# Performance work log

Hardware: AMD Instinct MI355X
Metric: run time of the kernel (lower is better)

The kernel has to match this reference:

```python
import jax, jax.numpy as jnp
import numpy as np

DIM = 512

def setup_inputs() -> dict:
    key = jax.random.key(0)
    ks = jax.random.split(key, 7)
    S = 8192
    scale = 1.0 / np.sqrt(DIM)
    x = jax.random.normal(ks[0], (S, DIM), dtype=jnp.float32)
    # torch.nn.Linear params: weight [out, in], bias [out]
    Wq = jax.random.uniform(ks[1], (DIM, DIM), jnp.float32, -scale, scale)
    bq = jax.random.uniform(ks[2], (DIM,), jnp.float32, -scale, scale)
    Wk = jax.random.uniform(ks[3], (DIM, DIM), jnp.float32, -scale, scale)
    bk = jax.random.uniform(ks[4], (DIM,), jnp.float32, -scale, scale)
    Wv = jax.random.uniform(ks[5], (DIM, DIM), jnp.float32, -scale, scale)
    bv = jax.random.uniform(ks[6], (DIM,), jnp.float32, -scale, scale)
    return {"x": x, "Wq": Wq, "bq": bq, "Wk": Wk, "bk": bk, "Wv": Wv, "bv": bv}

def reference(x, Wq, bq, Wk, bk, Wv, bv):
    S = x.shape[0]
    q = x @ Wq.T + bq  # [S, D]
    k = x @ Wk.T + bk
    v = x @ Wv.T + bv
    scores = (q @ k.T) / jnp.sqrt(jnp.asarray(DIM, x.dtype))  # [S, S]
    causal = jnp.tril(jnp.ones((S, S), dtype=bool))  # keep lower triangle incl. diag
    scores = jnp.where(causal, scores, -jnp.inf)
    attn_weights = jax.nn.softmax(scores, axis=-1)
    output = attn_weights @ v  # [S, D]
    return (output, attn_weights)
```

## Files before the change

### kernel.cpp

```cpp
#include <hip/hip_runtime.h>
#include <hip/hip_bf16.h>
#include <stdint.h>

#define S 8192
#define D 512
#define SCALE 0.044194173824159216f
#define KSPLIT 8

typedef __attribute__((ext_vector_type(8))) short short8;
typedef __attribute__((ext_vector_type(4))) float f32x4;

__device__ inline unsigned short f32_to_bf16(float f) {
    union { float f; uint32_t u; } v; v.f = f;
    uint32_t u = v.u;
    uint32_t r = (u + 0x7FFFu + ((u >> 16) & 1u)) >> 16;
    return (unsigned short)r;
}

__device__ inline uint2 pack4(float4 v) {
    uint2 p;
    p.x = (uint32_t)f32_to_bf16(v.x) | ((uint32_t)f32_to_bf16(v.y) << 16);
    p.y = (uint32_t)f32_to_bf16(v.z) | ((uint32_t)f32_to_bf16(v.w) << 16);
    return p;
}

__global__ __launch_bounds__(256) void k_convert(
    const float* __restrict__ x, const float* __restrict__ Wq,
    const float* __restrict__ Wk, const float* __restrict__ Wv,
    short* __restrict__ xb, short* __restrict__ Wb) {
    size_t i4 = (size_t)blockIdx.x * 256 + threadIdx.x;
    const size_t XN4 = (size_t)S * D / 4;
    if (i4 < XN4) {
        float4 v = reinterpret_cast<const float4*>(x)[i4];
        reinterpret_cast<uint2*>(xb)[i4] = pack4(v);
    } else {
        size_t j4 = i4 - XN4;
        size_t w = j4 >> 16;
        size_t rem = j4 & 65535;
        const float* src = (w == 0) ? Wq : ((w == 1) ? Wk : Wv);
        float4 v = reinterpret_cast<const float4*>(src)[rem];
        reinterpret_cast<uint2*>(Wb)[j4] = pack4(v);
    }
}

__device__ inline void stage_bf16(const short* __restrict__ src, int ld, short* dst, int t) {
#pragma unroll
    for (int j = 0; j < 2; j++) {
        int c = t + j * 256;
        int r = c >> 2;
        int kc = (c & 3) * 8;
        uint4 v = *reinterpret_cast<const uint4*>(&src[(size_t)r * ld + kc]);
        *reinterpret_cast<uint4*>(&dst[r * 32 + kc]) = v;
    }
}

__device__ inline void mfma_tile(const short* As, const short* Bs,
                                 f32x4 acc[4][4], int wr, int wc, int lane) {
    int rl = lane & 15;
    int kg = lane >> 4;
    short8 a[4], b[4];
#pragma unroll
    for (int m = 0; m < 4; m++)
        a[m] = *reinterpret_cast<const short8*>(&As[(wr * 64 + m * 16 + rl) * 32 + kg * 8]);
#pragma unroll
    for (int n = 0; n < 4; n++)
        b[n] = *reinterpret_cast<const short8*>(&Bs[(wc * 64 + n * 16 + rl) * 32 + kg * 8]);
#pragma unroll
    for (int m = 0; m < 4; m++)
#pragma unroll
        for (int n = 0; n < 4; n++)
            acc[m][n] = __builtin_amdgcn_mfma_f32_16x16x32_bf16(a[m], b[n], acc[m][n], 0, 0, 0);
}

__global__ __launch_bounds__(256) void k_qkv(
    const short* __restrict__ xb, const short* __restrict__ Wb,
    const float* __restrict__ bq, const float* __restrict__ bk,
    const float* __restrict__ bv, short* __restrict__ QKV) {
    __shared__ short As[128 * 32], Bs[128 * 32];
    int which = blockIdx.z;
    const short* W = Wb + (size_t)which * D * D;
    const float* bias = (which == 0) ? bq : ((which == 1) ? bk : bv);
    short* out = QKV + (size_t)which * S * D;
    int r0 = blockIdx.x * 128, c0 = blockIdx.y * 128;
    int t = threadIdx.x, lane = t & 63, w = t >> 6, wr = w >> 1, wc = w & 1;
    f32x4 acc[4][4];
#pragma unroll
    for (int m = 0; m < 4; m++)
#pragma unroll
        for (int n = 0; n < 4; n++)
#pragma unroll
            for (int j = 0; j < 4; j++) acc[m][n][j] = 0.0f;

    for (int kk = 0; kk < D; kk += 32) {
        __syncthreads();
        stage_bf16(xb + (size_t)r0 * D + kk, D, As, t);
        stage_bf16(W + (size_t)c0 * D + kk, D, Bs, t);
        __syncthreads();
        mfma_tile(As, Bs, acc, wr, wc, lane);
    }
    int rg = lane >> 4, cl = lane & 15;
#pragma unroll
    for (int m = 0; m < 4; m++)
#pragma unroll
        for (int n = 0; n < 4; n++) {
            int col = c0 + wc * 64 + n * 16 + cl;
            float b = bias[col];
#pragma unroll
            for (int j = 0; j < 4; j++) {
                int row = r0 + wr * 64 + m * 16 + rg * 4 + j;
                out[(size_t)row * D + col] = (short)f32_to_bf16(acc[m][n][j] + b);
            }
        }
}

__global__ __launch_bounds__(256) void k_transpose(const short* __restrict__ V,
                                                   short* __restrict__ Vt) {
    __shared__ short tile[64][65];
    int r0 = blockIdx.x * 64;
    int c0 = blockIdx.y * 64;
    int t = threadIdx.x;
#pragma unroll
    for (int j = 0; j < 16; j++) {
        int idx = t + j * 256;
        int r = idx >> 6, c = idx & 63;
        tile[r][c] = V[(size_t)(r0 + r) * D + c0 + c];
    }
    __syncthreads();
#pragma unroll
    for (int j = 0; j < 16; j++) {
        int idx = t + j * 256;
        int rr = idx >> 6, cc = idx & 63;
        Vt[(size_t)(c0 + rr) * S + r0 + cc] = tile[cc][rr];
    }
}

__global__ __launch_bounds__(256) void k_scores(const short* __restrict__ Qb,
                                                const short* __restrict__ Kb,
                                                float* __restrict__ attn) {
    int bj = blockIdx.x, bi = blockIdx.y;
    int r0 = bi * 128, c0 = bj * 128;
    int t = threadIdx.x;
    if (bj > bi) {
#pragma unroll
        for (int j = 0; j < 16; j++) {
            int c = t + j * 256;
            int r = c >> 5;
            int c4 = (c & 31) * 4;
            *reinterpret_cast<float4*>(&attn[(size_t)(r0 + r) * S + c0 + c4]) =
                make_float4(0.f, 0.f, 0.f, 0.f);
        }
        return;
    }
    __shared__ short As[128 * 32], Bs[128 * 32];
    int lane = t & 63, w = t >> 6, wr = w >> 1, wc = w & 1;
    f32x4 acc[4][4];
#pragma unroll
    for (int m = 0; m < 4; m++)
#pragma unroll
        for (int n = 0; n < 4; n++)
#pragma unroll
            for (int j = 0; j < 4; j++) acc[m][n][j] = 0.0f;

    for (int kk = 0; kk < D; kk += 32) {
        __syncthreads();
        stage_bf16(Qb + (size_t)r0 * D + kk, D, As, t);
        stage_bf16(Kb + (size_t)c0 * D + kk, D, Bs, t);
        __syncthreads();
        mfma_tile(As, Bs, acc, wr, wc, lane);
    }
    int rg = lane >> 4, cl = lane & 15;
#pragma unroll
    for (int m = 0; m < 4; m++)
#pragma unroll
        for (int n = 0; n < 4; n++) {
            int col = c0 + wc * 64 + n * 16 + cl;
#pragma unroll
            for (int j = 0; j < 4; j++) {
                int row = r0 + wr * 64 + m * 16 + rg * 4 + j;
                float v = acc[m][n][j] * SCALE;
                if (col > row) v = 0.0f;
                attn[(size_t)row * S + col] = v;
            }
        }
}

__global__ __launch_bounds__(256) void k_softmax(float* __restrict__ attn) {
    __shared__ float buf[S];
    __shared__ float red[16];
    int i = blockIdx.x;
    int t = threadIdx.x;
    int n = i + 1;
    float m = -__builtin_inff();
    for (int j = t; j < n; j += 256) {
        float v = attn[(size_t)i * S + j];
        buf[j] = v;
        m = fmaxf(m, v);
    }
#pragma unroll
    for (int o = 32; o > 0; o >>= 1) m = fmaxf(m, __shfl_xor(m, o, 64));
    int wid = t >> 6, lane = t & 63;
    if (lane == 0) red[wid] = m;
    __syncthreads();
    if (t == 0) {
        float mm = fmaxf(fmaxf(red[0], red[1]), fmaxf(red[2], red[3]));
        red[8] = mm;
    }
    __syncthreads();
    float M = red[8];
    float s = 0.f;
    for (int j = t; j < n; j += 256) {
        float e = __expf(buf[j] - M);
        buf[j] = e;
        s += e;
    }
#pragma unroll
    for (int o = 32; o > 0; o >>= 1) s += __shfl_xor(s, o, 64);
    __syncthreads();
    if (lane == 0) red[wid] = s;
    __syncthreads();
    if (t == 0) red[9] = 1.0f / (red[0] + red[1] + red[2] + red[3]);
    __syncthreads();
    float inv = red[9];
    for (int j = t; j < n; j += 256) attn[(size_t)i * S + j] = buf[j] * inv;
}

__global__ __launch_bounds__(256) void k_pv(const float* __restrict__ attn,
                                            const short* __restrict__ Vt,
                                            float* __restrict__ out) {
    int bn = blockIdx.x;
    int bi = blockIdx.y;
    int kz = blockIdx.z;
    int nsteps = (bi + 1) * 4;
    int per = (nsteps + KSPLIT - 1) / KSPLIT;
    int st0 = kz * per, st1 = min(nsteps, st0 + per);
    if (st0 >= st1) return;
    __shared__ short As[128 * 32], Bs[128 * 32];
    int r0 = bi * 128, c0 = bn * 128;
    int t = threadIdx.x, lane = t & 63, w = t >> 6, wr = w >> 1, wc = w & 1;
    f32x4 acc[4][4];
#pragma unroll
    for (int m = 0; m < 4; m++)
#pragma unroll
        for (int n = 0; n < 4; n++)
#pragma unroll
            for (int j = 0; j < 4; j++) acc[m][n][j] = 0.0f;

    for (int st = st0; st < st1; ++st) {
        int kk = st * 32;
        __syncthreads();
#pragma unroll
        for (int j = 0; j < 4; j++) {
            int c = t + j * 256;
            int r = c >> 3;
            int kc = (c & 7) * 4;
            float4 v = *reinterpret_cast<const float4*>(&attn[(size_t)(r0 + r) * S + kk + kc]);
            *reinterpret_cast<uint2*>(&As[r * 32 + kc]) = pack4(v);
        }
#pragma unroll
        for (int j = 0; j < 2; j++) {
            int c = t + j * 256;
            int r = c >> 2;
            int kc = (c & 3) * 8;
            uint4 v = *reinterpret_cast<const uint4*>(&Vt[(size_t)(c0 + r) * S + kk + kc]);
            *reinterpret_cast<uint4*>(&Bs[r * 32 + kc]) = v;
        }
        __syncthreads();
        mfma_tile(As, Bs, acc, wr, wc, lane);
    }
    int rg = lane >> 4, cl = lane & 15;
#pragma unroll
    for (int m = 0; m < 4; m++)
#pragma unroll
        for (int n = 0; n < 4; n++) {
            int col = c0 + wc * 64 + n * 16 + cl;
#pragma unroll
            for (int j = 0; j < 4; j++) {
                int row = r0 + wr * 64 + m * 16 + rg * 4 + j;
                atomicAdd(&out[(size_t)row * D + col], acc[m][n][j]);
            }
        }
}

extern "C" void kernel_launch(void* const* d_in, const int* in_sizes, int n_in,
                              void* d_out, int out_size, void* d_ws, size_t ws_size,
                              hipStream_t stream) {
    const float* x  = (const float*)d_in[0];
    const float* Wq = (const float*)d_in[1];
    const float* bq = (const float*)d_in[2];
    const float* Wk = (const float*)d_in[3];
    const float* bk = (const float*)d_in[4];
    const float* Wv = (const float*)d_in[5];
    const float* bv = (const float*)d_in[6];
    float* out  = (float*)d_out;
    float* attn = out + (size_t)S * D;

    short* xb  = (short*)d_ws;
    short* Wb  = xb + (size_t)S * D;
    short* QKV = Wb + (size_t)3 * D * D;
    short* Vt  = QKV + (size_t)3 * S * D;
    const short* Qb = QKV;
    const short* Kb = QKV + (size_t)S * D;
    const short* Vb = QKV + (size_t)2 * S * D;

    {
        size_t total4 = (size_t)S * D / 4 + (size_t)3 * D * D / 4;
        k_convert<<<dim3((unsigned)(total4 / 256)), 256, 0, stream>>>(x, Wq, Wk, Wv, xb, Wb);
    }
    k_qkv<<<dim3(S / 128, D / 128, 3), 256, 0, stream>>>(xb, Wb, bq, bk, bv, QKV);
    k_transpose<<<dim3(S / 64, D / 64), 256, 0, stream>>>(Vb, Vt);
    k_scores<<<dim3(S / 128, S / 128), 256, 0, stream>>>(Qb, Kb, attn);
    k_softmax<<<dim3(S), 256, 0, stream>>>(attn);
    hipMemsetAsync(d_out, 0, (size_t)S * D * sizeof(float), stream);
    k_pv<<<dim3(D / 128, S / 128, KSPLIT), 256, 0, stream>>>(attn, Vt, out);
}
```

Baseline: 575.3 us.

## Fuse softmax into scores and PV kernels using per-tile max/sum partials

```diff
diff --git a/kernel.cpp b/kernel.cpp
--- a/kernel.cpp
+++ b/kernel.cpp
@@ -5,7 +5,8 @@
 #define S 8192
 #define D 512
 #define SCALE 0.044194173824159216f
-#define KSPLIT 8
+#define KZ 4
+#define NEG_BIG -1e30f
 
 typedef __attribute__((ext_vector_type(8))) short short8;
 typedef __attribute__((ext_vector_type(4))) float f32x4;
@@ -22,6 +23,40 @@
     p.x = (uint32_t)f32_to_bf16(v.x) | ((uint32_t)f32_to_bf16(v.y) << 16);
     p.y = (uint32_t)f32_to_bf16(v.z) | ((uint32_t)f32_to_bf16(v.w) << 16);
     return p;
+}
+
+__device__ inline void gload16(const void* g, void* l) {
+    __builtin_amdgcn_global_load_lds(
+        (const __attribute__((address_space(1))) unsigned int*)g,
+        (__attribute__((address_space(3))) unsigned int*)l, 16, 0, 0);
+}
+
+__device__ inline void stage_g2l(const short* __restrict__ src, int ld, short* dst, int t) {
+    int w = t >> 6, l = t & 63;
+    int lr = l >> 2, lc = (l & 3) * 8;
+#pragma unroll
+    for (int j = 0; j < 2; j++) {
+        int row = (w << 5) + (j << 4) + lr;
+        gload16(src + (size_t)row * ld + lc, dst + (w << 10) + (j << 9));
+    }
+}
+
+__device__ inline void mfma_tile(const short* As, const short* Bs,
+                                 f32x4 acc[4][4], int wr, int wc, int lane) {
+    int rl = lane & 15;
+    int kg = lane >> 4;
+    short8 a[4], b[4];
+#pragma unroll
+    for (int m = 0; m < 4; m++)
+        a[m] = *reinterpret_cast<const short8*>(&As[(wr * 64 + m * 16 + rl) * 32 + kg * 8]);
+#pragma unroll
+    for (int n = 0; n < 4; n++)
+        b[n] = *reinterpret_cast<const short8*>(&Bs[(wc * 64 + n * 16 + rl) * 32 + kg * 8]);
+#pragma unroll
+    for (int m = 0; m < 4; m++)
+#pragma unroll
+        for (int n = 0; n < 4; n++)
+            acc[m][n] = __builtin_amdgcn_mfma_f32_16x16x32_bf16(a[m], b[n], acc[m][n], 0, 0, 0);
 }
 
 __global__ __launch_bounds__(256) void k_convert(
@@ -43,40 +78,11 @@
     }
 }
 
-__device__ inline void stage_bf16(const short* __restrict__ src, int ld, short* dst, int t) {
-#pragma unroll
-    for (int j = 0; j < 2; j++) {
-        int c = t + j * 256;
-        int r = c >> 2;
-        int kc = (c & 3) * 8;
-        uint4 v = *reinterpret_cast<const uint4*>(&src[(size_t)r * ld + kc]);
-        *reinterpret_cast<uint4*>(&dst[r * 32 + kc]) = v;
-    }
-}
-
-__device__ inline void mfma_tile(const short* As, const short* Bs,
-                                 f32x4 acc[4][4], int wr, int wc, int lane) {
-    int rl = lane & 15;
-    int kg = lane >> 4;
-    short8 a[4], b[4];
-#pragma unroll
-    for (int m = 0; m < 4; m++)
-        a[m] = *reinterpret_cast<const short8*>(&As[(wr * 64 + m * 16 + rl) * 32 + kg * 8]);
-#pragma unroll
-    for (int n = 0; n < 4; n++)
-        b[n] = *reinterpret_cast<const short8*>(&Bs[(wc * 64 + n * 16 + rl) * 32 + kg * 8]);
-#pragma unroll
-    for (int m = 0; m < 4; m++)
-#pragma unroll
-        for (int n = 0; n < 4; n++)
-            acc[m][n] = __builtin_amdgcn_mfma_f32_16x16x32_bf16(a[m], b[n], acc[m][n], 0, 0, 0);
-}
-
 __global__ __launch_bounds__(256) void k_qkv(
     const short* __restrict__ xb, const short* __restrict__ Wb,
     const float* __restrict__ bq, const float* __restrict__ bk,
     const float* __restrict__ bv, short* __restrict__ QKV) {
-    __shared__ short As[128 * 32], Bs[128 * 32];
+    __shared__ __align__(16) short As[128 * 32], Bs[128 * 32];
     int which = blockIdx.z;
     const short* W = Wb + (size_t)which * D * D;
     const float* bias = (which == 0) ? bq : ((which == 1) ? bk : bv);
@@ -93,8 +99,8 @@
 
     for (int kk = 0; kk < D; kk += 32) {
         __syncthreads();
-        stage_bf16(xb + (size_t)r0 * D + kk, D, As, t);
-        stage_bf16(W + (size_t)c0 * D + kk, D, Bs, t);
+        stage_g2l(xb + (size_t)r0 * D + kk, D, As, t);
+        stage_g2l(W + (size_t)c0 * D + kk, D, Bs, t);
         __syncthreads();
         mfma_tile(As, Bs, acc, wr, wc, lane);
     }
@@ -136,7 +142,10 @@
 
 __global__ __launch_bounds__(256) void k_scores(const short* __restrict__ Qb,
                                                 const short* __restrict__ Kb,
-                                                float* __restrict__ attn) {
+                                                float* __restrict__ raw,
+                                                float* __restrict__ attn,
+                                                float* __restrict__ pm,
+                                                float* __restrict__ pl) {
     int bj = blockIdx.x, bi = blockIdx.y;
     int r0 = bi * 128, c0 = bj * 128;
     int t = threadIdx.x;
@@ -151,7 +160,8 @@
         }
         return;
     }
-    __shared__ short As[128 * 32], Bs[128 * 32];
+    __shared__ __align__(16) short As[128 * 32], Bs[128 * 32];
+    __shared__ float wred[2][128], wsum[2][128];
     int lane = t & 63, w = t >> 6, wr = w >> 1, wc = w & 1;
     f32x4 acc[4][4];
 #pragma unroll
@@ -163,80 +173,103 @@
 
     for (int kk = 0; kk < D; kk += 32) {
         __syncthreads();
-        stage_bf16(Qb + (size_t)r0 * D + kk, D, As, t);
-        stage_bf16(Kb + (size_t)c0 * D + kk, D, Bs, t);
+        stage_g2l(Qb + (size_t)r0 * D + kk, D, As, t);
+        stage_g2l(Kb + (size_t)c0 * D + kk, D, Bs, t);
         __syncthreads();
         mfma_tile(As, Bs, acc, wr, wc, lane);
     }
     int rg = lane >> 4, cl = lane & 15;
+    bool diag = (bi == bj);
+#pragma unroll
+    for (int m = 0; m < 4; m++)
+#pragma unroll
+        for (int n = 0; n < 4; n++)
+#pragma unroll
+            for (int jj = 0; jj < 4; jj++) {
+                int row = wr * 64 + m * 16 + rg * 4 + jj;
+                int col = wc * 64 + n * 16 + cl;
+                float v = acc[m][n][jj] * SCALE;
+                if (diag && col > row) v = NEG_BIG;
+                acc[m][n][jj] = v;
+            }
+#pragma unroll
+    for (int m = 0; m < 4; m++)
+#pragma unroll
+        for (int jj = 0; jj < 4; jj++) {
+            float x = fmaxf(fmaxf(acc[m][0][jj], acc[m][1][jj]),
+                            fmaxf(acc[m][2][jj], acc[m][3][jj]));
+#pragma unroll
+            for (int o = 1; o < 16; o <<= 1) x = fmaxf(x, __shfl_xor(x, o, 64));
+            if (cl == 0) wred[wc][wr * 64 + m * 16 + rg * 4 + jj] = x;
+        }
+    __syncthreads();
+#pragma unroll
+    for (int m = 0; m < 4; m++)
+#pragma unroll
+        for (int jj = 0; jj < 4; jj++) {
+            int rloc = wr * 64 + m * 16 + rg * 4 + jj;
+            float mr = fmaxf(wred[0][rloc], wred[1][rloc]);
+            float sse = __expf(acc[m][0][jj] - mr) + __expf(acc[m][1][jj] - mr) +
+                        __expf(acc[m][2][jj] - mr) + __expf(acc[m][3][jj] - mr);
+#pragma unroll
+            for (int o = 1; o < 16; o <<= 1) sse += __shfl_xor(sse, o, 64);
+            if (cl == 0) wsum[wc][rloc] = sse;
+        }
 #pragma unroll
     for (int m = 0; m < 4; m++)
 #pragma unroll
         for (int n = 0; n < 4; n++) {
             int col = c0 + wc * 64 + n * 16 + cl;
 #pragma unroll
-            for (int j = 0; j < 4; j++) {
-                int row = r0 + wr * 64 + m * 16 + rg * 4 + j;
-                float v = acc[m][n][j] * SCALE;
-                if (col > row) v = 0.0f;
-                attn[(size_t)row * S + col] = v;
+            for (int jj = 0; jj < 4; jj++) {
+                int row = r0 + wr * 64 + m * 16 + rg * 4 + jj;
+                raw[(size_t)row * S + col] = acc[m][n][jj];
             }
         }
-}
-
-__global__ __launch_bounds__(256) void k_softmax(float* __restrict__ attn) {
-    __shared__ float buf[S];
-    __shared__ float red[16];
-    int i = blockIdx.x;
+    __syncthreads();
+    if (t < 128) {
+        float mr = fmaxf(wred[0][t], wred[1][t]);
+        pm[(size_t)bj * S + r0 + t] = mr;
+        pl[(size_t)bj * S + r0 + t] = wsum[0][t] + wsum[1][t];
+    }
+}
+
+__global__ __launch_bounds__(256) void k_combine(const float* __restrict__ pm,
+                                                 const float* __restrict__ pl,
+                                                 float* __restrict__ M,
+                                                 float* __restrict__ Li) {
+    int row = blockIdx.x * 256 + threadIdx.x;
+    int nt = (row >> 7) + 1;
+    float m = -3e38f;
+    for (int j = 0; j < nt; j++) m = fmaxf(m, pm[(size_t)j * S + row]);
+    float l = 0.f;
+    for (int j = 0; j < nt; j++) l += pl[(size_t)j * S + row] * __expf(pm[(size_t)j * S + row] - m);
+    M[row] = m;
+    Li[row] = 1.0f / l;
+}
+
+__global__ __launch_bounds__(512) void k_pvnorm(const float* __restrict__ raw,
+                                                const short* __restrict__ Vt,
+                                                const float* __restrict__ M,
+                                                const float* __restrict__ Li,
+                                                float* __restrict__ attn,
+                                                float* __restrict__ out) {
+    int idx = blockIdx.x;
+    int panel = 63 - (idx & 63);
+    int rest = idx >> 6;
+    int bn = rest & 1;
+    int kz = rest >> 1;
+    int r0 = panel * 128;
     int t = threadIdx.x;
-    int n = i + 1;
-    float m = -__builtin_inff();
-    for (int j = t; j < n; j += 256) {
-        float v = attn[(size_t)i * S + j];
-        buf[j] = v;
-        m = fmaxf(m, v);
-    }
-#pragma unroll
-    for (int o = 32; o > 0; o >>= 1) m = fmaxf(m, __shfl_xor(m, o, 64));
-    int wid = t >> 6, lane = t & 63;
-    if (lane == 0) red[wid] = m;
-    __syncthreads();
-    if (t == 0) {
-        float mm = fmaxf(fmaxf(red[0], red[1]), fmaxf(red[2], red[3]));
-        red[8] = mm;
-    }
-    __syncthreads();
-    float M = red[8];
-    float s = 0.f;
-    for (int j = t; j < n; j += 256) {
-        float e = __expf(buf[j] - M);
-        buf[j] = e;
-        s += e;
-    }
-#pragma unroll
-    for (int o = 32; o > 0; o >>= 1) s += __shfl_xor(s, o, 64);
-    __syncthreads();
-    if (lane == 0) red[wid] = s;
-    __syncthreads();
-    if (t == 0) red[9] = 1.0f / (red[0] + red[1] + red[2] + red[3]);
-    __syncthreads();
-    float inv = red[9];
-    for (int j = t; j < n; j += 256) attn[(size_t)i * S + j] = buf[j] * inv;
-}
-
-__global__ __launch_bounds__(256) void k_pv(const float* __restrict__ attn,
-                                            const short* __restrict__ Vt,
-                                            float* __restrict__ out) {
-    int bn = blockIdx.x;
-    int bi = blockIdx.y;
-    int kz = blockIdx.z;
-    int nsteps = (bi + 1) * 4;
-    int per = (nsteps + KSPLIT - 1) / KSPLIT;
-    int st0 = kz * per, st1 = min(nsteps, st0 + per);
+    int nst = (panel + 1) * 4;
+    int per = (nst + KZ - 1) / KZ;
+    int st0 = kz * per, st1 = min(nst, st0 + per);
     if (st0 >= st1) return;
-    __shared__ short As[128 * 32], Bs[128 * 32];
-    int r0 = bi * 128, c0 = bn * 128;
-    int t = threadIdx.x, lane = t & 63, w = t >> 6, wr = w >> 1, wc = w & 1;
+    __shared__ __align__(16) short As[128 * 32];
+    __shared__ __align__(16) short Bs[256 * 32];
+    __shared__ float Ml[128], Ll[128];
+    if (t < 128) { Ml[t] = M[r0 + t]; Ll[t] = Li[r0 + t]; }
+    int lane = t & 63, w = t >> 6, wr = w >> 2, wc = w & 3;
     f32x4 acc[4][4];
 #pragma unroll
     for (int m = 0; m < 4; m++)
@@ -245,25 +278,26 @@
 #pragma unroll
             for (int j = 0; j < 4; j++) acc[m][n][j] = 0.0f;
 
+    const short* vbase = Vt + (size_t)(bn * 256) * S;
     for (int st = st0; st < st1; ++st) {
         int kk = st * 32;
         __syncthreads();
 #pragma unroll
-        for (int j = 0; j < 4; j++) {
-            int c = t + j * 256;
-            int r = c >> 3;
-            int kc = (c & 7) * 4;
-            float4 v = *reinterpret_cast<const float4*>(&attn[(size_t)(r0 + r) * S + kk + kc]);
-            *reinterpret_cast<uint2*>(&As[r * 32 + kc]) = pack4(v);
-        }
-#pragma unroll
         for (int j = 0; j < 2; j++) {
-            int c = t + j * 256;
-            int r = c >> 2;
-            int kc = (c & 3) * 8;
-            uint4 v = *reinterpret_cast<const uint4*>(&Vt[(size_t)(c0 + r) * S + kk + kc]);
-            *reinterpret_cast<uint4*>(&Bs[r * 32 + kc]) = v;
-        }
+            int c = t + j * 512;
+            int r = c >> 3, kc = (c & 7) * 4;
+            float4 v = *reinterpret_cast<const float4*>(&raw[(size_t)(r0 + r) * S + kk + kc]);
+            float mlr = Ml[r], llr = Ll[r];
+            float4 p;
+            p.x = __expf(v.x - mlr) * llr;
+            p.y = __expf(v.y - mlr) * llr;
+            p.z = __expf(v.z - mlr) * llr;
+            p.w = __expf(v.w - mlr) * llr;
+            if (bn == 0)
+                *reinterpret_cast<float4*>(&attn[(size_t)(r0 + r) * S + kk + kc]) = p;
+            *reinterpret_cast<uint2*>(&As[r * 32 + kc]) = pack4(p);
+        }
+        stage_g2l(vbase + kk, S, Bs, t);
         __syncthreads();
         mfma_tile(As, Bs, acc, wr, wc, lane);
     }
@@ -272,11 +306,11 @@
     for (int m = 0; m < 4; m++)
 #pragma unroll
         for (int n = 0; n < 4; n++) {
-            int col = c0 + wc * 64 + n * 16 + cl;
-#pragma unroll
-            for (int j = 0; j < 4; j++) {
-                int row = r0 + wr * 64 + m * 16 + rg * 4 + j;
-                atomicAdd(&out[(size_t)row * D + col], acc[m][n][j]);
+            int col = bn * 256 + wc * 64 + n * 16 + cl;
+#pragma unroll
+            for (int jj = 0; jj < 4; jj++) {
+                int row = r0 + wr * 64 + m * 16 + rg * 4 + jj;
+                atomicAdd(&out[(size_t)row * D + col], acc[m][n][jj]);
             }
         }
 }
@@ -298,6 +332,12 @@
     short* Wb  = xb + (size_t)S * D;
     short* QKV = Wb + (size_t)3 * D * D;
     short* Vt  = QKV + (size_t)3 * S * D;
+    float* raw = (float*)(Vt + (size_t)S * D);
+    float* pm  = raw + (size_t)S * S;
+    float* pl  = pm + (size_t)64 * S;
+    float* M   = pl + (size_t)64 * S;
+    float* Li  = M + S;
+
     const short* Qb = QKV;
     const short* Kb = QKV + (size_t)S * D;
     const short* Vb = QKV + (size_t)2 * S * D;
@@ -308,8 +348,8 @@
     }
     k_qkv<<<dim3(S / 128, D / 128, 3), 256, 0, stream>>>(xb, Wb, bq, bk, bv, QKV);
     k_transpose<<<dim3(S / 64, D / 64), 256, 0, stream>>>(Vb, Vt);
-    k_scores<<<dim3(S / 128, S / 128), 256, 0, stream>>>(Qb, Kb, attn);
-    k_softmax<<<dim3(S), 256, 0, stream>>>(attn);
+    k_scores<<<dim3(S / 128, S / 128), 256, 0, stream>>>(Qb, Kb, raw, attn, pm, pl);
+    k_combine<<<dim3(S / 256), 256, 0, stream>>>(pm, pl, M, Li);
     hipMemsetAsync(d_out, 0, (size_t)S * D * sizeof(float), stream);
-    k_pv<<<dim3(D / 128, S / 128, KSPLIT), 256, 0, stream>>>(attn, Vt, out);
-}
+    k_pvnorm<<<dim3(2 * 64 * KZ), 512, 0, stream>>>(raw, Vt, M, Li, attn, out);
+}
```

New measurement: 588.2 us. 1.02x slower.
